# Performance work log

Hardware: AMD Instinct MI355X
Metric: run time of the kernel (lower is better)

## Reference

```python
import jax, jax.numpy as jnp
import numpy as np

V = 50000      # dxVocabSize
NA = 10000     # dxnumAncestors
NR = 16        # dxnumRelations
D = 128        # dxEmbDim
A = 128        # attnDim
L = 8          # ancestors per leaf segment


def setup_inputs() -> dict:
    key = jax.random.key(0)
    ks = jax.random.split(key, 16)
    s = 0.05
    return {
        "dxEmb": jax.random.normal(ks[0], (V + 1, D), jnp.float32) * s,
        "classEmb": jax.random.normal(ks[1], (V + 1, D), jnp.float32) * s,
        "reEmb": jax.random.normal(ks[2], (NR + 1, D), jnp.float32) * s,
        "anEmbTab": jax.random.normal(ks[3], (V + NA + 1, D), jnp.float32) * s,
        "W1": jax.random.normal(ks[4], (2 * D, A), jnp.float32) * s,
        "b1": jax.random.normal(ks[5], (A,), jnp.float32) * s,
        "W2": jax.random.normal(ks[6], (A, 1), jnp.float32) * s,
        "b2": jax.random.normal(ks[7], (1,), jnp.float32) * s,
        "Wc": jax.random.normal(ks[8], (D, 1), jnp.float32) * s,
        "bc": jax.random.normal(ks[9], (1,), jnp.float32) * s,
        "leaves": jax.random.randint(ks[10], (V, L), 0, V + 1),
        "ancestors": jax.random.randint(ks[11], (V, L), 0, V + NA + 1),
        "relations": jax.random.randint(ks[12], (V, L), 0, NR + 1),
        "permute_index": jax.random.permutation(ks[13], V + 1),
    }


def reference(dxEmb, classEmb, reEmb, anEmbTab, W1, b1, W2, b2, Wc, bc,
              leaves, ancestors, relations, permute_index):
    # Per-segment gathers, vectorized over all V leaf segments at once.
    relE = reEmb[relations]                       # [V,L,D]
    leavesE = dxEmb[leaves]                       # [V,L,D]
    # class coefficient from the first leaf of each segment
    class_coe = classEmb[leaves[:, 0]] @ Wc + bc  # [V,1]
    relE = class_coe[:, :, None] * relE           # [V,L,D]
    anc = anEmbTab[ancestors]                     # [V,L,D]
    msg = anc + relE                              # [V,L,D]
    attn_in = jnp.concatenate([leavesE, msg], axis=-1)   # [V,L,2D]
    mlp = jnp.tanh(attn_in @ W1 + b1)             # [V,L,A]
    pre = mlp @ W2 + b2                           # [V,L,1]
    # Faithful to original: F.softmax(preAttn, dim=1) on a [L,1] tensor
    # normalizes over the trailing size-1 axis (yields ones).
    attn = jax.nn.softmax(pre, axis=-1)           # [V,L,1]
    temp = jnp.sum(msg * attn, axis=1)            # [V,D]
    all_emb = jnp.concatenate([temp, jnp.zeros((1, D), temp.dtype)], axis=0)  # [V+1,D]
    return all_emb[permute_index]
```

## Files before the change

### kernel.cpp

```cpp
#include <hip/hip_runtime.h>


#define RG_V  50000
#define RG_L  8

typedef float f32x4_native __attribute__((ext_vector_type(4)));

__device__ __forceinline__ float4 f4add(float4 a, float4 b) {
    return make_float4(a.x + b.x, a.y + b.y, a.z + b.z, a.w + b.w);
}
__device__ __forceinline__ float4 f4fma(float s, float4 a, float4 b) {
    return make_float4(fmaf(s, a.x, b.x), fmaf(s, a.y, b.y),
                       fmaf(s, a.z, b.z), fmaf(s, a.w, b.w));
}
__device__ __forceinline__ float4 shfl_xor32_f4(float4 x) {
    return make_float4(__shfl_xor(x.x, 32, 64), __shfl_xor(x.y, 32, 64),
                       __shfl_xor(x.z, 32, 64), __shfl_xor(x.w, 32, 64));
}

__global__ __launch_bounds__(256) void rgat_fused_kernel(
    const float* __restrict__ classEmb,
    const float* __restrict__ reEmb,
    const float* __restrict__ anEmbTab,
    const float* __restrict__ Wc,
    const float* __restrict__ bc,
    const int*  __restrict__ leaves,
    const int*  __restrict__ ancestors,
    const int*  __restrict__ relations,
    const int*  __restrict__ perm,
    float*      __restrict__ out)
{
    const int wid  = blockIdx.x * 4 + (threadIdx.x >> 6);
    const int row0 = wid * 2;
    if (row0 > RG_V) return;
    const int lane = threadIdx.x & 63;
    const int h    = lane >> 5;
    const int li   = lane & 31;
    const bool have1 = (row0 + 1 <= RG_V);

    const int p0 = perm[row0];
    const int p1 = have1 ? perm[row0 + 1] : 0;
    const bool valid0 = (p0 < RG_V);
    const bool valid1 = have1 && (p1 < RG_V);
    const int v0 = valid0 ? p0 : 0;
    const int v1 = valid1 ? p1 : 0;

    const int4* anc4 = reinterpret_cast<const int4*>(ancestors);
    const int4* rel4 = reinterpret_cast<const int4*>(relations);
    const int4 a00 = anc4[v0 * 2], a01 = anc4[v0 * 2 + 1];
    const int4 a10 = anc4[v1 * 2], a11 = anc4[v1 * 2 + 1];
    const int4 r00 = rel4[v0 * 2], r01 = rel4[v0 * 2 + 1];
    const int4 r10 = rel4[v1 * 2], r11 = rel4[v1 * 2 + 1];
    const int lv0 = leaves[v0 * RG_L];
    const int lv1 = leaves[v1 * RG_L];

    const int ia00 = h ? a00.y : a00.x, ia01 = h ? a00.w : a00.z;
    const int ia02 = h ? a01.y : a01.x, ia03 = h ? a01.w : a01.z;
    const int ia10 = h ? a10.y : a10.x, ia11 = h ? a10.w : a10.z;
    const int ia12 = h ? a11.y : a11.x, ia13 = h ? a11.w : a11.z;
    const int ir00 = h ? r00.y : r00.x, ir01 = h ? r00.w : r00.z;
    const int ir02 = h ? r01.y : r01.x, ir03 = h ? r01.w : r01.z;
    const int ir10 = h ? r10.y : r10.x, ir11 = h ? r10.w : r10.z;
    const int ir12 = h ? r11.y : r11.x, ir13 = h ? r11.w : r11.z;

    const float4* anT = reinterpret_cast<const float4*>(anEmbTab);
    const float4* reT = reinterpret_cast<const float4*>(reEmb);
    const float4* clT = reinterpret_cast<const float4*>(classEmb);
    const float4* wcT = reinterpret_cast<const float4*>(Wc);

    const float4 gA00 = anT[(size_t)ia00 * 32 + li];
    const float4 gA01 = anT[(size_t)ia01 * 32 + li];
    const float4 gA02 = anT[(size_t)ia02 * 32 + li];
    const float4 gA03 = anT[(size_t)ia03 * 32 + li];
    const float4 gA10 = anT[(size_t)ia10 * 32 + li];
    const float4 gA11 = anT[(size_t)ia11 * 32 + li];
    const float4 gA12 = anT[(size_t)ia12 * 32 + li];
    const float4 gA13 = anT[(size_t)ia13 * 32 + li];
    const float4 gR00 = reT[(size_t)ir00 * 32 + li];
    const float4 gR01 = reT[(size_t)ir01 * 32 + li];
    const float4 gR02 = reT[(size_t)ir02 * 32 + li];
    const float4 gR03 = reT[(size_t)ir03 * 32 + li];
    const float4 gR10 = reT[(size_t)ir10 * 32 + li];
    const float4 gR11 = reT[(size_t)ir11 * 32 + li];
    const float4 gR12 = reT[(size_t)ir12 * 32 + li];
    const float4 gR13 = reT[(size_t)ir13 * 32 + li];
    const float4 c4 = clT[(size_t)(h ? lv1 : lv0) * 32 + li];
    const float4 w4 = wcT[li];

    float4 accA0 = f4add(f4add(gA00, gA01), f4add(gA02, gA03));
    float4 accA1 = f4add(f4add(gA10, gA11), f4add(gA12, gA13));
    float4 accR0 = f4add(f4add(gR00, gR01), f4add(gR02, gR03));
    float4 accR1 = f4add(f4add(gR10, gR11), f4add(gR12, gR13));

    float part = c4.x * w4.x + c4.y * w4.y + c4.z * w4.z + c4.w * w4.w;
    #pragma unroll
    for (int off = 16; off >= 1; off >>= 1)
        part += __shfl_xor(part, off, 64);
    const float coe = part + bc[0];

    float4 oxA = shfl_xor32_f4(h ? accA0 : accA1);
    float4 oxR = shfl_xor32_f4(h ? accR0 : accR1);
    float4 myA = f4add(h ? accA1 : accA0, oxA);
    float4 myR = f4add(h ? accR1 : accR0, oxR);

    float4 res = f4fma(coe, myR, myA);
    const bool validOwn = h ? valid1 : valid0;
    if (!validOwn) res = make_float4(0.f, 0.f, 0.f, 0.f);

    if (h == 0 || have1) {
        float4* dst = reinterpret_cast<float4*>(out) + (size_t)row0 * 32 + lane;
        __builtin_nontemporal_store(*reinterpret_cast<f32x4_native*>(&res),
                                    reinterpret_cast<f32x4_native*>(dst));
    }
}

extern "C" void kernel_launch(void* const* d_in, const int* in_sizes, int n_in,
                              void* d_out, int out_size, void* d_ws, size_t ws_size,
                              hipStream_t stream) {
    const float* classEmb  = (const float*)d_in[1];
    const float* reEmb     = (const float*)d_in[2];
    const float* anEmbTab  = (const float*)d_in[3];
    const float* Wc        = (const float*)d_in[8];
    const float* bc        = (const float*)d_in[9];
    const int*   leaves    = (const int*)d_in[10];
    const int*   ancestors = (const int*)d_in[11];
    const int*   relations = (const int*)d_in[12];
    const int*   perm      = (const int*)d_in[13];
    float*       out       = (float*)d_out;

    const int waves  = (RG_V + 1 + 1) / 2;
    const int blocks = (waves + 3) / 4;

    rgat_fused_kernel<<<blocks, 256, 0, stream>>>(
        classEmb, reEmb, anEmbTab, Wc, bc,
        leaves, ancestors, relations, perm, out);
}
```

Before: 155.2 us.

## Precompute class coefficients in separate kernel and stage relation table in LDS

```diff
diff --git a/kernel.cpp b/kernel.cpp
--- a/kernel.cpp
+++ b/kernel.cpp
@@ -3,6 +3,7 @@
 
 #define RG_V  50000
 #define RG_L  8
+#define RG_NR 17
 
 typedef float f32x4_native __attribute__((ext_vector_type(4)));
 
@@ -18,18 +19,43 @@
                        __shfl_xor(x.z, 32, 64), __shfl_xor(x.w, 32, 64));
 }
 
-__global__ __launch_bounds__(256) void rgat_fused_kernel(
+__global__ __launch_bounds__(256) void rgat_coe_kernel(
     const float* __restrict__ classEmb,
+    const float* __restrict__ Wc,
+    const float* __restrict__ bc,
+    float*       __restrict__ coeTab)
+{
+    const int row = blockIdx.x * 4 + (threadIdx.x >> 6);
+    if (row > RG_V) return;
+    const int lane = threadIdx.x & 63;
+    const float2 c = reinterpret_cast<const float2*>(classEmb)[row * 64 + lane];
+    const float2 w = reinterpret_cast<const float2*>(Wc)[lane];
+    float p = c.x * w.x + c.y * w.y;
+    #pragma unroll
+    for (int off = 32; off >= 1; off >>= 1)
+        p += __shfl_xor(p, off, 64);
+    if (lane == 0) coeTab[row] = p + bc[0];
+}
+
+__global__ __launch_bounds__(256) void rgat_main_kernel(
     const float* __restrict__ reEmb,
     const float* __restrict__ anEmbTab,
-    const float* __restrict__ Wc,
-    const float* __restrict__ bc,
+    const float* __restrict__ coeTab,
     const int*  __restrict__ leaves,
     const int*  __restrict__ ancestors,
     const int*  __restrict__ relations,
     const int*  __restrict__ perm,
     float*      __restrict__ out)
 {
+    __shared__ float reSh[RG_NR * 128];
+
+    {
+        const float4* src = reinterpret_cast<const float4*>(reEmb);
+        float4*       dst = reinterpret_cast<float4*>(reSh);
+        for (int i = threadIdx.x; i < RG_NR * 32; i += 256) dst[i] = src[i];
+    }
+    __syncthreads();
+
     const int wid  = blockIdx.x * 4 + (threadIdx.x >> 6);
     const int row0 = wid * 2;
     if (row0 > RG_V) return;
@@ -64,9 +90,7 @@
     const int ir12 = h ? r11.y : r11.x, ir13 = h ? r11.w : r11.z;
 
     const float4* anT = reinterpret_cast<const float4*>(anEmbTab);
-    const float4* reT = reinterpret_cast<const float4*>(reEmb);
-    const float4* clT = reinterpret_cast<const float4*>(classEmb);
-    const float4* wcT = reinterpret_cast<const float4*>(Wc);
+    const float4* reS = reinterpret_cast<const float4*>(reSh);
 
     const float4 gA00 = anT[(size_t)ia00 * 32 + li];
     const float4 gA01 = anT[(size_t)ia01 * 32 + li];
@@ -76,27 +100,22 @@
     const float4 gA11 = anT[(size_t)ia11 * 32 + li];
     const float4 gA12 = anT[(size_t)ia12 * 32 + li];
     const float4 gA13 = anT[(size_t)ia13 * 32 + li];
-    const float4 gR00 = reT[(size_t)ir00 * 32 + li];
-    const float4 gR01 = reT[(size_t)ir01 * 32 + li];
-    const float4 gR02 = reT[(size_t)ir02 * 32 + li];
-    const float4 gR03 = reT[(size_t)ir03 * 32 + li];
-    const float4 gR10 = reT[(size_t)ir10 * 32 + li];
-    const float4 gR11 = reT[(size_t)ir11 * 32 + li];
-    const float4 gR12 = reT[(size_t)ir12 * 32 + li];
-    const float4 gR13 = reT[(size_t)ir13 * 32 + li];
-    const float4 c4 = clT[(size_t)(h ? lv1 : lv0) * 32 + li];
-    const float4 w4 = wcT[li];
+
+    const float coe = coeTab[h ? lv1 : lv0];
+
+    const float4 gR00 = reS[ir00 * 32 + li];
+    const float4 gR01 = reS[ir01 * 32 + li];
+    const float4 gR02 = reS[ir02 * 32 + li];
+    const float4 gR03 = reS[ir03 * 32 + li];
+    const float4 gR10 = reS[ir10 * 32 + li];
+    const float4 gR11 = reS[ir11 * 32 + li];
+    const float4 gR12 = reS[ir12 * 32 + li];
+    const float4 gR13 = reS[ir13 * 32 + li];
 
     float4 accA0 = f4add(f4add(gA00, gA01), f4add(gA02, gA03));
     float4 accA1 = f4add(f4add(gA10, gA11), f4add(gA12, gA13));
     float4 accR0 = f4add(f4add(gR00, gR01), f4add(gR02, gR03));
     float4 accR1 = f4add(f4add(gR10, gR11), f4add(gR12, gR13));
-
-    float part = c4.x * w4.x + c4.y * w4.y + c4.z * w4.z + c4.w * w4.w;
-    #pragma unroll
-    for (int off = 16; off >= 1; off >>= 1)
-        part += __shfl_xor(part, off, 64);
-    const float coe = part + bc[0];
 
     float4 oxA = shfl_xor32_f4(h ? accA0 : accA1);
     float4 oxR = shfl_xor32_f4(h ? accR0 : accR1);
@@ -127,11 +146,16 @@
     const int*   relations = (const int*)d_in[12];
     const int*   perm      = (const int*)d_in[13];
     float*       out       = (float*)d_out;
+    float*       coeTab    = (float*)d_ws;
 
-    const int waves  = (RG_V + 1 + 1) / 2;
-    const int blocks = (waves + 3) / 4;
-
-    rgat_fused_kernel<<<blocks, 256, 0, stream>>>(
-        classEmb, reEmb, anEmbTab, Wc, bc,
-        leaves, ancestors, relations, perm, out);
+    {
+        const int blocks = (RG_V + 1 + 3) / 4;
+        rgat_coe_kernel<<<blocks, 256, 0, stream>>>(classEmb, Wc, bc, coeTab);
+    }
+    {
+        const int waves  = (RG_V + 1 + 1) / 2;
+        const int blocks = (waves + 3) / 4;
+        rgat_main_kernel<<<blocks, 256, 0, stream>>>(
+            reEmb, anEmbTab, coeTab, leaves, ancestors, relations, perm, out);
+    }
 }
```

New measurement: 160.8 us. 3.7% more time.
